# Kernel optimization log

Measured on AMD Instinct MI355X. Metric: run time of the kernel, lower is better.

## Reference

```python
import jax, jax.numpy as jnp
import numpy as np

N = 20000      # nodes / tokens
H = 256        # hidden_size
NH = 8         # num_heads
HD = NH * H    # num_heads * hidden_size = 2048
EPS = 1e-5


def setup_inputs() -> dict:
    key = jax.random.key(0)
    ks = jax.random.split(key, 24)

    def lin_w(k, i, o):
        # xavier-ish scale for a Linear weight stored as [in, out]
        return jax.random.normal(k, (i, o), jnp.float32) * (1.0 / np.sqrt(i))

    inp = {
        'q': jax.random.normal(ks[0], (N, H), jnp.float32),
        'k': jax.random.normal(ks[1], (N, H), jnp.float32),
        'v': jax.random.normal(ks[2], (N, H), jnp.float32),
        'layer': 1,
        'Wq1': lin_w(ks[3], H, HD), 'bq1': jnp.zeros((HD,), jnp.float32),
        'Wk1': lin_w(ks[4], H, HD), 'bk1': jnp.zeros((HD,), jnp.float32),
        'Wq2': lin_w(ks[5], H, HD), 'bq2': jnp.zeros((HD,), jnp.float32),
        'Wk2': lin_w(ks[6], H, HD), 'bk2': jnp.zeros((HD,), jnp.float32),
        'Wv':  lin_w(ks[7], H, HD), 'bv':  jnp.zeros((HD,), jnp.float32),
        'ln_g': jnp.ones((HD,), jnp.float32),
        'ln_b': jnp.zeros((HD,), jnp.float32),
        'Wo': lin_w(ks[8], HD, H), 'bo': jnp.zeros((H,), jnp.float32),
        'lq1': jax.random.normal(ks[9], (H,), jnp.float32) * 0.1,
        'lk1': jax.random.normal(ks[10], (H,), jnp.float32) * 0.1,
        'lq2': jax.random.normal(ks[11], (H,), jnp.float32) * 0.1,
        'lk2': jax.random.normal(ks[12], (H,), jnp.float32) * 0.1,
    }
    return inp


def reference(q, k, v, layer, Wq1, bq1, Wk1, bk1, Wq2, bq2, Wk2, bk2,
              Wv, bv, ln_g, ln_b, Wo, bo, lq1, lk1, lq2, lk2):
    # projections: [N, H] -> [N, HD]
    q1 = q @ Wq1 + bq1
    k1 = k @ Wk1 + bk1
    q2 = q @ Wq2 + bq2
    k2 = k @ Wk2 + bk2
    vv = v @ Wv + bv

    # linear attention: K^T V -> [HD, HD]  (dropout is identity in eval mode)
    k1v = k1.T @ vv
    k2v = k2.T @ vv

    # lambda gating (scalars)
    lam1 = jnp.exp(jnp.sum(lq1 * lk1))
    lam2 = jnp.exp(jnp.sum(lq2 * lk2))
    lam_init = 0.8 - 0.6 * jnp.exp(jnp.asarray(-0.3 * layer, jnp.float32))
    lam_full = lam1 - lam2 + lam_init

    # Q @ (K^T V), differential subtraction: [N, HD]
    x = q1 @ k1v - lam_full * (q2 @ k2v)

    # LayerNorm over last dim (biased variance, eps=1e-5, like torch)
    mu = jnp.mean(x, axis=-1, keepdims=True)
    var = jnp.mean(jnp.square(x - mu), axis=-1, keepdims=True)
    x = (x - mu) / jnp.sqrt(var + EPS) * ln_g + ln_b

    x = x * (1.0 - lam_init)
    return x @ Wo + bo  # [N, H]
```

## Files before the change

### kernel.cpp

```cpp
#include <hip/hip_runtime.h>
#include <stdint.h>

typedef __bf16 bf16x8 __attribute__((ext_vector_type(8)));
typedef __bf16 bf16x4v __attribute__((ext_vector_type(4)));
typedef float f32x4 __attribute__((ext_vector_type(4)));
typedef float f32x2 __attribute__((ext_vector_type(2)));
typedef unsigned short u16x4 __attribute__((ext_vector_type(4)));
typedef unsigned short u16x8 __attribute__((ext_vector_type(8)));

#define NTOK 20000
#define NTP  20480
#define HIW  256
#define HD   2048
#define LDKP 66
#define LDS2 72
#define TSZ  16384

static __device__ __forceinline__ float bf2f(unsigned short h) {
  union { unsigned u; float f; } c; c.u = ((unsigned)h) << 16;
  return c.f;
}
static __device__ __forceinline__ unsigned short fbits(float x) {
  __bf16 h = (__bf16)x;
  return __builtin_bit_cast(unsigned short, h);
}

#define WRED(x) { x += __shfl_xor(x,32); x += __shfl_xor(x,16); x += __shfl_xor(x,8); \
                  x += __shfl_xor(x,4);  x += __shfl_xor(x,2);  x += __shfl_xor(x,1); }


__global__ __launch_bounds__(256) void k_front(
    const float* __restrict__ kk, const float* __restrict__ vv,
    const float* __restrict__ Wq1, const float* __restrict__ Wk1,
    const float* __restrict__ Wq2, const float* __restrict__ Wk2,
    const float* __restrict__ lq1, const float* __restrict__ lk1,
    const float* __restrict__ lq2, const float* __restrict__ lk2,
    const float* __restrict__ bq1, const float* __restrict__ bk1,
    const float* __restrict__ bq2, const float* __restrict__ bk2,
    const int* __restrict__ layer,
    unsigned short* __restrict__ kT, unsigned short* __restrict__ vT,
    float* __restrict__ skp, float* __restrict__ svp,
    unsigned short* __restrict__ Pc_part, float* __restrict__ scal,
    float* __restrict__ S) {
  __shared__ float SMEM[64][260];
  const int b = blockIdx.x, t = threadIdx.x;

  if (b < 640) {
    const int tile = b >> 1, m = b & 1;
    const float* src = m ? vv : kk;
    unsigned short* dstT = m ? vT : kT;
    float* sump = m ? svp : skp;
    #pragma unroll
    for (int i = 0; i < 16; ++i) {
      int ch = i * 256 + t;
      int row = ch >> 6, c4 = (ch & 63) * 4;
      int gtok = tile * 64 + row;
      f32x4 val = {0.f, 0.f, 0.f, 0.f};
      if (gtok < NTOK) val = *(const f32x4*)&src[(size_t)gtok * HIW + c4];
      *(f32x4*)&SMEM[row][c4] = val;
    }
    __syncthreads();
    float sum = 0.f;
    unsigned short cv[64];
    #pragma unroll
    for (int tok = 0; tok < 64; ++tok) {
      float x = SMEM[tok][t];
      sum += x;
      cv[tok] = fbits(x);
    }
    sump[tile * 256 + t] = sum;
    size_t base = (size_t)tile * TSZ + (size_t)t * 64;
    #pragma unroll
    for (int s = 0; s < 8; ++s)
      *(u16x8*)&dstT[base + s * 8] = *(const u16x8*)&cv[s * 8];
  } else if (b < 768) {
    unsigned short* Ak = (unsigned short*)SMEM;
    unsigned short* Bk = Ak + 128 * LDKP;
    const int idx = b - 640;
    const int pair = idx >> 6, rem = idx & 63;
    const int z = rem & 15, by = (rem >> 4) & 1, bx = (rem >> 5) & 1;
    const int i0 = bx * 128, j0 = by * 128;
    const int lane = t & 63, wave = t >> 6;
    const int wr = (wave >> 1) * 64, wc = (wave & 1) * 64;
    const int r15 = lane & 15, kg = (lane >> 4) * 8;
    const float* Wa = pair ? Wq2 : Wq1;
    const float* Wb = pair ? Wk2 : Wk1;
    f32x4 acc[4][4];
    #pragma unroll
    for (int m = 0; m < 4; ++m)
      #pragma unroll
      for (int n = 0; n < 4; ++n) acc[m][n] = (f32x4){0.f, 0.f, 0.f, 0.f};
    const int srow = t >> 1, sh = (t & 1) * 32;
    for (int kt = 0; kt < 2; ++kt) {
      const int kb = z * 128 + kt * 64 + sh;
      __syncthreads();
      #pragma unroll
      for (int c = 0; c < 8; ++c) {
        f32x4 a = *(const f32x4*)&Wa[(size_t)(i0 + srow) * HD + kb + c * 4];
        f32x4 bb = *(const f32x4*)&Wb[(size_t)(j0 + srow) * HD + kb + c * 4];
        bf16x4v oa, ob;
        #pragma unroll
        for (int u = 0; u < 4; ++u) { oa[u] = (__bf16)a[u]; ob[u] = (__bf16)bb[u]; }
        *(bf16x4v*)&Ak[srow * LDKP + sh + c * 4] = oa;
        *(bf16x4v*)&Bk[srow * LDKP + sh + c * 4] = ob;
      }
      __syncthreads();
      #pragma unroll
      for (int ks = 0; ks < 2; ++ks) {
        const int ko = ks * 32 + kg;
        bf16x8 ah[4], bh[4];
        #pragma unroll
        for (int m = 0; m < 4; ++m)
          ah[m] = *(const bf16x8*)&Ak[(wr + m * 16 + r15) * LDKP + ko];
        #pragma unroll
        for (int n = 0; n < 4; ++n)
          bh[n] = *(const bf16x8*)&Bk[(wc + n * 16 + r15) * LDKP + ko];
        #pragma unroll
        for (int m = 0; m < 4; ++m)
          #pragma unroll
          for (int n = 0; n < 4; ++n)
            acc[m][n] = __builtin_amdgcn_mfma_f32_16x16x32_bf16(ah[m], bh[n], acc[m][n], 0, 0, 0);
      }
    }
    const int rg = (lane >> 4) * 4;
    unsigned short* Pp = Pc_part + (size_t)(pair * 16 + z) * 65536;
    #pragma unroll
    for (int m = 0; m < 4; ++m)
      #pragma unroll
      for (int n = 0; n < 4; ++n)
        #pragma unroll
        for (int r = 0; r < 4; ++r)
          Pp[(i0 + wr + m * 16 + rg + r) * 256 + (j0 + wc + n * 16 + r15)] = fbits(acc[m][n][r]);
  } else if (b == 768) {
    float* red = (float*)SMEM;
    float p1 = lq1[t] * lk1[t], p2 = lq2[t] * lk2[t];
    float d1 = 0.f, d2 = 0.f;
    #pragma unroll
    for (int u = 0; u < 8; ++u) {
      d1 += bq1[t * 8 + u] * bk1[t * 8 + u];
      d2 += bq2[t * 8 + u] * bk2[t * 8 + u];
    }
    WRED(p1); WRED(p2); WRED(d1); WRED(d2);
    int w = t >> 6;
    if ((t & 63) == 0) { red[w] = p1; red[4 + w] = p2; red[8 + w] = d1; red[12 + w] = d2; }
    __syncthreads();
    if (t == 0) {
      float s1 = red[0] + red[1] + red[2] + red[3];
      float s2 = red[4] + red[5] + red[6] + red[7];
      float dd1 = red[8] + red[9] + red[10] + red[11];
      float dd2 = red[12] + red[13] + red[14] + red[15];
      float li = 0.8f - 0.6f * expf(-0.3f * (float)layer[0]);
      float lam = expf(s1) - expf(s2) + li;
      scal[0] = lam; scal[1] = -lam; scal[2] = 1.0f - li; scal[3] = li;
      scal[4] = dd1 - lam * dd2;
    }
  } else {
    const f32x4 z4 = {0.f, 0.f, 0.f, 0.f};
    #pragma unroll
    for (int i = 0; i < 64; ++i)
      *(f32x4*)&S[i * 1024 + t * 4] = z4;
  }
}

__global__ __launch_bounds__(512) void k_mid(
    const unsigned short* __restrict__ kT, const unsigned short* __restrict__ vT,
    float* __restrict__ S, const unsigned short* __restrict__ Pc_part,
    const float* __restrict__ skp, const float* __restrict__ svp,
    float* __restrict__ Pc, float* __restrict__ sk, float* __restrict__ sv,
    const float* __restrict__ Wk1, const float* __restrict__ Wk2,
    const float* __restrict__ Wq1, const float* __restrict__ Wq2,
    const float* __restrict__ bq1, const float* __restrict__ bq2,
    const float* __restrict__ bk1, const float* __restrict__ bk2,
    const float* __restrict__ scal, float* __restrict__ gc, float* __restrict__ uc) {
  __shared__ unsigned short SB[2 * 2 * 128 * LDS2];
  const int b = blockIdx.x, t = threadIdx.x;

  if (b < 256) {
    const int z = b & 63, by = (b >> 6) & 1, bx = (b >> 7) & 1;
    const int i0 = bx * 128, j0 = by * 128;
    const int lane = t & 63, wave = t >> 6;
    const int wr = (wave >> 1) * 32, wc = (wave & 1) * 64;
    const int r15 = lane & 15, kg = (lane >> 4) * 8;
    const int m = t >> 8;
    const int local = t & 255;
    const int row2 = local >> 1;
    const int koff = (local & 1) * 32;
    const unsigned short* srcT = m ? vT : kT;
    const size_t tbase = (size_t)(5 * z) * TSZ + (size_t)((m ? j0 : i0) + row2) * 64 + koff;
    const int lds_off = m * 128 * LDS2 + row2 * LDS2 + koff;

    f32x4 acc[2][4];
    #pragma unroll
    for (int mm = 0; mm < 2; ++mm)
      #pragma unroll
      for (int n = 0; n < 4; ++n) acc[mm][n] = (f32x4){0.f, 0.f, 0.f, 0.f};
    u16x8 rA[4], rB[4];

#define LOADT(R, KT)                                                          \
    { _Pragma("unroll")                                                       \
      for (int c = 0; c < 4; ++c)                                             \
        R[c] = *(const u16x8*)&srcT[tbase + (size_t)(KT) * TSZ + c * 8]; }
#define WRITET(BUF, R)                                                        \
    { unsigned short* d = &SB[(BUF) * 2 * 128 * LDS2 + lds_off];              \
      _Pragma("unroll")                                                       \
      for (int c = 0; c < 4; ++c) *(u16x8*)&d[c * 8] = R[c]; }

    LOADT(rA, 0)
    WRITET(0, rA)
    LOADT(rB, 1)
    asm volatile("s_waitcnt lgkmcnt(0)" ::: "memory");
    __builtin_amdgcn_s_barrier();

    #pragma unroll
    for (int kt = 0; kt < 5; ++kt) {
      const unsigned short* Ab = &SB[(kt & 1) * 2 * 128 * LDS2];
      const unsigned short* Bb = Ab + 128 * LDS2;
      __builtin_amdgcn_s_setprio(1);
      #pragma unroll
      for (int ks = 0; ks < 2; ++ks) {
        const int ko = ks * 32 + kg;
        bf16x8 ah[2], bh[4];
        #pragma unroll
        for (int mm = 0; mm < 2; ++mm)
          ah[mm] = *(const bf16x8*)&Ab[(wr + mm * 16 + r15) * LDS2 + ko];
        #pragma unroll
        for (int n = 0; n < 4; ++n)
          bh[n] = *(const bf16x8*)&Bb[(wc + n * 16 + r15) * LDS2 + ko];
        #pragma unroll
        for (int mm = 0; mm < 2; ++mm)
          #pragma unroll
          for (int n = 0; n < 4; ++n)
            acc[mm][n] = __builtin_amdgcn_mfma_f32_16x16x32_bf16(ah[mm], bh[n], acc[mm][n], 0, 0, 0);
      }
      __builtin_amdgcn_s_setprio(0);
      if (kt < 4) {
        if ((kt & 1) == 0) {
          WRITET(1, rB)
          if (kt + 2 <= 4) LOADT(rA, kt + 2)
        } else {
          WRITET(0, rA)
          if (kt + 2 <= 4) LOADT(rB, kt + 2)
        }
      }
      asm volatile("s_waitcnt lgkmcnt(0)" ::: "memory");
      __builtin_amdgcn_s_barrier();
    }
#undef LOADT
#undef WRITET
    const int rg = (lane >> 4) * 4;
    #pragma unroll
    for (int mm = 0; mm < 2; ++mm)
      #pragma unroll
      for (int n = 0; n < 4; ++n)
        #pragma unroll
        for (int r = 0; r < 4; ++r)
          atomicAdd(&S[(i0 + wr + mm * 16 + rg + r) * 256 + (j0 + wc + n * 16 + r15)],
                    acc[mm][n][r]);
  } else if (b < 288) {
    if (t < 256) {
      size_t idx = (size_t)(b - 256) * 2048 + t * 8;
      float s1[8] = {}, s2[8] = {};
      #pragma unroll 2
      for (int z = 0; z < 16; ++z) {
        u16x8 ha = *(const u16x8*)&Pc_part[(size_t)z * 65536 + idx];
        u16x8 hb = *(const u16x8*)&Pc_part[(size_t)(16 + z) * 65536 + idx];
        #pragma unroll
        for (int u = 0; u < 8; ++u) { s1[u] += bf2f(ha[u]); s2[u] += bf2f(hb[u]); }
      }
      float lam = scal[0];
      #pragma unroll
      for (int u = 0; u < 8; ++u) Pc[idx + u] = s1[u] - lam * s2[u];
    }
  } else if (b < 290) {
    if (t < 256) {
      const float* src = (b == 288) ? skp : svp;
      float s = 0.f;
      for (int z = 0; z < 320; ++z) s += src[z * 256 + t];
      if (b == 288) sk[t] = s; else sv[t] = s;
    }
  } else {
    if (t < 256) {
      int bb = b - 290, lane = t & 63, w = t >> 6;
      bool dogc = bb < 16;
      const float* A1 = dogc ? Wk1 : Wq1;
      const float* A2 = dogc ? Wk2 : Wq2;
      const float* x1 = dogc ? bq1 : bk1;
      const float* x2 = dogc ? bq2 : bk2;
      float* outv = dogc ? gc : uc;
      float lam = scal[0];
      int rb = (bb & 15) * 16 + w * 4;
      for (int q2 = 0; q2 < 4; ++q2) {
        int row = rb + q2;
        float s1 = 0.f, s2 = 0.f;
        #pragma unroll
        for (int c = 0; c < 8; ++c) {
          int kk2 = c * 256 + lane * 4;
          f32x4 a1 = *(const f32x4*)&A1[(size_t)row * HD + kk2];
          f32x4 a2 = *(const f32x4*)&A2[(size_t)row * HD + kk2];
          f32x4 v1 = *(const f32x4*)&x1[kk2];
          f32x4 v2 = *(const f32x4*)&x2[kk2];
          #pragma unroll
          for (int u = 0; u < 4; ++u) { s1 += a1[u] * v1[u]; s2 += a2[u] * v2[u]; }
        }
        WRED(s1); WRED(s2);
        if (lane == 0) outv[row] = s1 - lam * s2;
      }
    }
  }
}

__global__ __launch_bounds__(256) void k_ac(
    const float* __restrict__ Pc, const float* __restrict__ S,
    const float* __restrict__ gc, const float* __restrict__ sk,
    float* __restrict__ Ac, float* __restrict__ tc, float* __restrict__ rv,
    float* __restrict__ scal) {
  int b = blockIdx.x, t = threadIdx.x;
  if (b < 32) {
    __shared__ float Pt[32][68];
    __shared__ float St[64][68];
    int i0 = (b >> 2) * 32, j0 = (b & 3) * 64;
    int ti = t >> 5, tj = t & 31;
    float acc[4][2] = {};
    for (int kt = 0; kt < 256; kt += 64) {
      __syncthreads();
      {
        int rr = t >> 3, c8 = (t & 7) * 8;
        *(f32x4*)&Pt[rr][c8] = *(const f32x4*)&Pc[(i0 + rr) * 256 + kt + c8];
        *(f32x4*)&Pt[rr][c8 + 4] = *(const f32x4*)&Pc[(i0 + rr) * 256 + kt + c8 + 4];
      }
      {
        int rr = t >> 2, c16 = (t & 3) * 16;
        #pragma unroll
        for (int c = 0; c < 4; ++c)
          *(f32x4*)&St[rr][c16 + c * 4] = *(const f32x4*)&S[(kt + rr) * 256 + j0 + c16 + c * 4];
      }
      __syncthreads();
      #pragma unroll 8
      for (int k2 = 0; k2 < 64; ++k2) {
        float a[4];
        #pragma unroll
        for (int u = 0; u < 4; ++u) a[u] = Pt[ti * 4 + u][k2];
        f32x2 b2 = *(const f32x2*)&St[k2][tj * 2];
        #pragma unroll
        for (int u = 0; u < 4; ++u) { acc[u][0] += a[u] * b2[0]; acc[u][1] += a[u] * b2[1]; }
      }
    }
    #pragma unroll
    for (int u = 0; u < 4; ++u) {
      Ac[(i0 + ti * 4 + u) * 256 + j0 + tj * 2] = acc[u][0];
      Ac[(i0 + ti * 4 + u) * 256 + j0 + tj * 2 + 1] = acc[u][1];
    }
  } else if (b == 32) {
    int lane = t & 63, w = t >> 6;
    f32x4 sk4 = *(const f32x4*)&sk[lane * 4];
    for (int ii = 0; ii < 64; ++ii) {
      int i = w * 64 + ii;
      f32x4 p4 = *(const f32x4*)&Pc[i * 256 + lane * 4];
      float s = p4[0] * sk4[0] + p4[1] * sk4[1] + p4[2] * sk4[2] + p4[3] * sk4[3];
      WRED(s);
      if (lane == 0) tc[i] = s;
    }
  } else {
    float s0 = 0.f, s1 = 0.f, s2 = 0.f, s3 = 0.f;
    #pragma unroll 4
    for (int i = 0; i < 256; i += 4) {
      s0 += gc[i] * S[i * 256 + t];
      s1 += gc[i + 1] * S[(i + 1) * 256 + t];
      s2 += gc[i + 2] * S[(i + 2) * 256 + t];
      s3 += gc[i + 3] * S[(i + 3) * 256 + t];
    }
    rv[t] = (s0 + s1) + (s2 + s3);
    if (t < 64) {
      f32x4 g4 = *(const f32x4*)&gc[t * 4];
      f32x4 sk4 = *(const f32x4*)&sk[t * 4];
      float a = g4[0] * sk4[0] + g4[1] * sk4[1] + g4[2] * sk4[2] + g4[3] * sk4[3];
      WRED(a);
      if (t == 0) scal[5] = a;
    }
  }
}

__global__ __launch_bounds__(256) void k_gc(
    const float* __restrict__ Ac, const float* __restrict__ Wv,
    const float* __restrict__ tc, const float* __restrict__ uc,
    const float* __restrict__ sv, const float* __restrict__ rv,
    const float* __restrict__ bv, const float* __restrict__ scal,
    float* __restrict__ Gc, float* __restrict__ cc) {
  __shared__ float At[64][68];
  __shared__ float Bt[64][132];
  __shared__ float svr[256], rvr[256];
  int t = threadIdx.x;
  int i0 = blockIdx.x * 64, j0 = blockIdx.y * 128;
  int ti = t >> 5, tj = t & 31;
  svr[t] = sv[t]; rvr[t] = rv[t];
  float acc[8][4] = {};
  f32x4 swa = {0.f, 0.f, 0.f, 0.f}, sca = {0.f, 0.f, 0.f, 0.f};
  for (int kt = 0; kt < 256; kt += 64) {
    __syncthreads();
    {
      int rr = t >> 2, c16 = (t & 3) * 16;
      #pragma unroll
      for (int c = 0; c < 4; ++c)
        *(f32x4*)&At[rr][c16 + c * 4] = *(const f32x4*)&Ac[(i0 + rr) * 256 + kt + c16 + c * 4];
    }
    {
      int rr = t >> 2, c32 = (t & 3) * 32;
      #pragma unroll
      for (int c = 0; c < 8; ++c)
        *(f32x4*)&Bt[rr][c32 + c * 4] = *(const f32x4*)&Wv[(size_t)(kt + rr) * HD + j0 + c32 + c * 4];
    }
    __syncthreads();
    #pragma unroll 8
    for (int k2 = 0; k2 < 64; ++k2) {
      float a[8];
      #pragma unroll
      for (int u = 0; u < 8; ++u) a[u] = At[ti * 8 + u][k2];
      f32x4 b = *(const f32x4*)&Bt[k2][tj * 4];
      float svk = svr[kt + k2], rvk = rvr[kt + k2];
      swa += b * svk; sca += b * rvk;
      #pragma unroll
      for (int u = 0; u < 8; ++u)
        #pragma unroll
        for (int v = 0; v < 4; ++v) acc[u][v] += a[u] * b[v];
    }
  }
  int j = j0 + tj * 4;
  f32x4 bv4 = *(const f32x4*)&bv[j];
  f32x4 wnb;
  #pragma unroll
  for (int v = 0; v < 4; ++v) wnb[v] = swa[v] + 20000.0f * bv4[v];
  if (blockIdx.x == 0 && ti == 0) {
    float ac = scal[5], dc = scal[4];
    f32x4 ccv;
    #pragma unroll
    for (int v = 0; v < 4; ++v) ccv[v] = sca[v] + ac * bv4[v] + dc * wnb[v];
    *(f32x4*)&cc[j] = ccv;
  }
  #pragma unroll
  for (int u = 0; u < 8; ++u) {
    int i = i0 + ti * 8 + u;
    float tci = tc[i], uci = uc[i];
    f32x4 o;
    #pragma unroll
    for (int v = 0; v < 4; ++v)
      o[v] = acc[u][v] + tci * bv4[v] + uci * wnb[v];
    *(f32x4*)&Gc[(size_t)i * HD + j] = o;
  }
}

__global__ __launch_bounds__(256) void k_post(
    const float* __restrict__ Gc, const float* __restrict__ cc,
    const float* __restrict__ Wo, const float* __restrict__ g,
    const float* __restrict__ lnb, const float* __restrict__ scal_c,
    unsigned short* __restrict__ Bt2, float* __restrict__ M_part,
    float* __restrict__ Hc_part, float* __restrict__ scal) {
  __shared__ float SMEM[8768];
  int b = blockIdx.x, t = threadIdx.x;
  if (b < 17) {
    int lane = t & 63, w = t >> 6;
    if (b < 16) {
      int rb = b * 16 + w * 4;
      for (int q2 = 0; q2 < 4; ++q2) {
        int row = rb + q2;
        float s1 = 0.f, s2 = 0.f;
        #pragma unroll
        for (int c = 0; c < 8; ++c) {
          int kk2 = c * 256 + lane * 4;
          f32x4 g4 = *(const f32x4*)&Gc[(size_t)row * HD + kk2];
          f32x4 c4v = *(const f32x4*)&cc[kk2];
          #pragma unroll
          for (int u = 0; u < 4; ++u) { s1 += g4[u]; s2 += g4[u] * c4v[u]; }
        }
        WRED(s1); WRED(s2);
        if (lane == 0) {
          int base = ((256 + (row >> 5)) * 64 + ((row >> 3) & 3) * 16) * 8 + (row & 7);
          Bt2[base] = fbits(s1 * (1.0f / 2048.0f));
          Bt2[base + 8] = fbits(s2);
        }
      }
    } else {
      float s1 = 0.f, s2 = 0.f;
      #pragma unroll
      for (int c = 0; c < 2; ++c) {
        f32x4 v = *(const f32x4*)&cc[t * 8 + c * 4];
        #pragma unroll
        for (int u = 0; u < 4; ++u) { s1 += v[u]; s2 += v[u] * v[u]; }
      }
      WRED(s1); WRED(s2);
      if ((t & 63) == 0) { SMEM[t >> 6] = s1; SMEM[4 + (t >> 6)] = s2; }
      __syncthreads();
      if (t == 0) {
        scal[6] = SMEM[4] + SMEM[5] + SMEM[6] + SMEM[7];
        scal[7] = (SMEM[0] + SMEM[1] + SMEM[2] + SMEM[3]) * (1.0f / 2048.0f);
      }
      for (int idx = t; idx < 14 * 256; idx += 256) {
        int ci = idx >> 8, kk2 = idx & 255;
        int col = 514 + ci;
        Bt2[((256 + (kk2 >> 5)) * 64 + ((kk2 >> 3) & 3) * 16 + (col & 15)) * 8 + (kk2 & 7)] = 0;
      }
    }
  } else if (b < 81) {
    float (*Gi)[68] = (float(*)[68])SMEM;
    float (*Gj)[69] = (float(*)[69])(SMEM + 64 * 68);
    int idx = b - 17;
    int bx = idx & 3, by = (idx >> 2) & 3, z = idx >> 4;
    int i0 = bx * 64, j0 = by * 64;
    int ti = t >> 5, tj = t & 31;
    float acc[8][2] = {};
    for (int kt = 0; kt < 512; kt += 64) {
      int kb = z * 512 + kt;
      __syncthreads();
      {
        int rr = t >> 2, c16 = (t & 3) * 16;
        #pragma unroll
        for (int c = 0; c < 4; ++c) {
          *(f32x4*)&Gi[rr][c16 + c * 4] = *(const f32x4*)&Gc[(size_t)(i0 + rr) * HD + kb + c16 + c * 4];
          *(f32x4*)&Gj[rr][c16 + c * 4] = *(const f32x4*)&Gc[(size_t)(j0 + rr) * HD + kb + c16 + c * 4];
        }
      }
      __syncthreads();
      #pragma unroll 8
      for (int k2 = 0; k2 < 64; ++k2) {
        float a[8];
        #pragma unroll
        for (int u = 0; u < 8; ++u) a[u] = Gi[ti * 8 + u][k2];
        float b0 = Gj[tj * 2][k2], b1 = Gj[tj * 2 + 1][k2];
        #pragma unroll
        for (int u = 0; u < 8; ++u) { acc[u][0] += a[u] * b0; acc[u][1] += a[u] * b1; }
      }
    }
    #pragma unroll
    for (int u = 0; u < 8; ++u) {
      M_part[(size_t)z * 65536 + (i0 + ti * 8 + u) * 256 + j0 + tj * 2] = acc[u][0];
      M_part[(size_t)z * 65536 + (i0 + ti * 8 + u) * 256 + j0 + tj * 2 + 1] = acc[u][1];
    }
  } else {
    float (*At)[68] = (float(*)[68])SMEM;
    float (*Bt)[68] = (float(*)[68])(SMEM + 32 * 68);
    int idx = b - 81;
    int bx = idx % 9, rem = idx / 9, by = rem & 3, z = rem >> 2;
    int i0 = bx * 32, j0 = by * 64;
    float s2 = scal_c[2];
    int ti = t >> 5, tj = t & 31;
    float acc[4][2] = {};
    for (int kt = 0; kt < 512; kt += 64) {
      int kb = z * 512 + kt;
      __syncthreads();
      {
        int rr = t >> 3, c8 = (t & 7) * 8, gi = i0 + rr;
        #pragma unroll
        for (int h = 0; h < 8; h += 4) {
          f32x4 g4 = *(const f32x4*)&g[kb + c8 + h];
          f32x4 a;
          if (gi < 256) {
            f32x4 gg = *(const f32x4*)&Gc[(size_t)gi * HD + kb + c8 + h];
            #pragma unroll
            for (int u = 0; u < 4; ++u) a[u] = gg[u] * g4[u];
          } else if (gi == 256) {
            a = g4;
          } else if (gi == 257) {
            f32x4 c4v = *(const f32x4*)&cc[kb + c8 + h];
            #pragma unroll
            for (int u = 0; u < 4; ++u) a[u] = c4v[u] * g4[u];
          } else if (gi == 258) {
            a = *(const f32x4*)&lnb[kb + c8 + h];
          } else {
            a = (f32x4){0.f, 0.f, 0.f, 0.f};
          }
          *(f32x4*)&At[rr][c8 + h] = a;
        }
      }
      {
        int rr = t >> 2, c16 = (t & 3) * 16;
        #pragma unroll
        for (int c = 0; c < 4; ++c) {
          f32x4 bb = *(const f32x4*)&Wo[(size_t)(kb + rr) * 256 + j0 + c16 + c * 4];
          #pragma unroll
          for (int u = 0; u < 4; ++u) bb[u] *= s2;
          *(f32x4*)&Bt[rr][c16 + c * 4] = bb;
        }
      }
      __syncthreads();
      #pragma unroll 8
      for (int k2 = 0; k2 < 64; ++k2) {
        float a[4];
        #pragma unroll
        for (int u = 0; u < 4; ++u) a[u] = At[ti * 4 + u][k2];
        f32x2 b2 = *(const f32x2*)&Bt[k2][tj * 2];
        #pragma unroll
        for (int u = 0; u < 4; ++u) { acc[u][0] += a[u] * b2[0]; acc[u][1] += a[u] * b2[1]; }
      }
    }
    #pragma unroll
    for (int u = 0; u < 4; ++u) {
      Hc_part[(size_t)z * 73728 + (i0 + ti * 4 + u) * 256 + j0 + tj * 2] = acc[u][0];
      Hc_part[(size_t)z * 73728 + (i0 + ti * 4 + u) * 256 + j0 + tj * 2 + 1] = acc[u][1];
    }
  }
}

__global__ __launch_bounds__(256) void k_red2(
    const float* __restrict__ M_part, const float* __restrict__ Hc_part,
    const float* __restrict__ bo, unsigned short* __restrict__ Bt2,
    float* __restrict__ wbar, float* __restrict__ hcv, float* __restrict__ bcv) {
  int bi = blockIdx.x, z2 = blockIdx.y, t = threadIdx.x;
  if (z2 == 2) {
    if (bi != 0) return;
    float s0 = 0.f, s1 = 0.f, s2 = 0.f;
    #pragma unroll
    for (int z = 0; z < 4; ++z) {
      s0 += Hc_part[(size_t)z * 73728 + 256 * 256 + t];
      s1 += Hc_part[(size_t)z * 73728 + 257 * 256 + t];
      s2 += Hc_part[(size_t)z * 73728 + 258 * 256 + t];
    }
    wbar[t] = s0; hcv[t] = s1; bcv[t] = s2 + bo[t];
    return;
  }
  __shared__ unsigned short T[64][256];
  const float* src = z2 ? Hc_part : M_part;
  const size_t sp = z2 ? 73728 : 65536;
  const int base = z2 ? 256 : 0;
  for (int ii = 0; ii < 64; ++ii) {
    int i = bi * 64 + ii;
    float s = 0.f;
    #pragma unroll
    for (int z = 0; z < 4; ++z) s += src[z * sp + i * 256 + t];
    T[ii][t] = fbits(s);
  }
  __syncthreads();
  const int col = base + t;
  #pragma unroll
  for (int c = 0; c < 64; c += 8) {
    u16x8 o;
    #pragma unroll
    for (int u = 0; u < 8; ++u) o[u] = T[c + u][t];
    int kk0 = bi * 64 + c;
    int addr = (((col >> 4) * 8 + (kk0 >> 5)) * 64 + ((kk0 >> 3) & 3) * 16 + (col & 15)) * 8;
    *(u16x8*)&Bt2[addr] = o;
  }
}

__global__ __launch_bounds__(512) void k_out(
    const float* __restrict__ q, const unsigned short* __restrict__ Bt2,
    const float* __restrict__ hcv, const float* __restrict__ wbar,
    const float* __restrict__ bcv, const float* __restrict__ scal,
    float* __restrict__ out) {
  __shared__ unsigned short As[32 * 264];
  __shared__ float zbuf[32][260];
  __shared__ float sqp[4][32];
  __shared__ float muL[32], m2L[32];
  const int t = threadIdx.x, lane = t & 63, wave = t >> 6;
  const int row0 = blockIdx.x * 32;
  const int r15 = lane & 15, kg = lane >> 4;
  {
    #pragma unroll
    for (int i = 0; i < 4; ++i) {
      int ch = i * 512 + t;
      int row = ch >> 6, c4 = (ch & 63) * 4;
      f32x4 v = *(const f32x4*)&q[(size_t)(row0 + row) * HIW + c4];
      bf16x4v o;
      #pragma unroll
      for (int u = 0; u < 4; ++u) o[u] = (__bf16)v[u];
      *(bf16x4v*)&As[row * 264 + c4] = o;
    }
  }
  __syncthreads();
  const bool isM = wave < 4;
  const int wcol = isM ? wave * 64 : 256 + (wave - 4) * 64;
  const int grp0 = wcol >> 4;
  f32x4 acc[2][5];
  #pragma unroll
  for (int m = 0; m < 2; ++m)
    #pragma unroll
    for (int n = 0; n < 5; ++n) acc[m][n] = (f32x4){0.f, 0.f, 0.f, 0.f};
  __builtin_amdgcn_s_setprio(1);
  #pragma unroll
  for (int ko = 0; ko < 8; ++ko) {
    bf16x8 af0 = *(const bf16x8*)&As[r15 * 264 + ko * 32 + kg * 8];
    bf16x8 af1 = *(const bf16x8*)&As[(16 + r15) * 264 + ko * 32 + kg * 8];
    #pragma unroll
    for (int ni = 0; ni < 5; ++ni) {
      if (ni == 4 && wave != 7) continue;
      const int grp = (ni == 4) ? 32 : grp0 + ni;
      bf16x8 bfr = *(const bf16x8*)&Bt2[(size_t)(grp * 8 + ko) * 512 + lane * 8];
      acc[0][ni] = __builtin_amdgcn_mfma_f32_16x16x32_bf16(af0, bfr, acc[0][ni], 0, 0, 0);
      acc[1][ni] = __builtin_amdgcn_mfma_f32_16x16x32_bf16(af1, bfr, acc[1][ni], 0, 0, 0);
    }
  }
  __builtin_amdgcn_s_setprio(0);
  if (isM) {
    #pragma unroll
    for (int m = 0; m < 2; ++m)
      #pragma unroll
      for (int r = 0; r < 4; ++r) {
        int rowl = m * 16 + kg * 4 + r;
        float p = 0.f;
        #pragma unroll
        for (int ni = 0; ni < 4; ++ni) {
          int col = wcol + ni * 16 + r15;
          p += acc[m][ni][r] * bf2f(As[rowl * 264 + col]);
        }
        p += __shfl_xor(p, 1); p += __shfl_xor(p, 2);
        p += __shfl_xor(p, 4); p += __shfl_xor(p, 8);
        if (r15 == 0) sqp[wave][rowl] = p;
      }
  } else {
    #pragma unroll
    for (int m = 0; m < 2; ++m)
      #pragma unroll
      for (int r = 0; r < 4; ++r) {
        int rowl = m * 16 + kg * 4 + r;
        #pragma unroll
        for (int ni = 0; ni < 4; ++ni)
          zbuf[rowl][(wcol - 256) + ni * 16 + r15] = acc[m][ni][r];
      }
    if (wave == 7) {
      #pragma unroll
      for (int m = 0; m < 2; ++m)
        #pragma unroll
        for (int r = 0; r < 4; ++r) {
          int rowl = m * 16 + kg * 4 + r;
          if (r15 == 0) muL[rowl] = acc[m][4][r];
          if (r15 == 1) m2L[rowl] = acc[m][4][r];
        }
    }
  }
  __syncthreads();
  const float css = scal[6], cbar = scal[7];
  #pragma unroll
  for (int i = 0; i < 4; ++i) {
    const int row = i * 8 + wave;
    const int c4 = lane * 4;
    float mu = muL[row] + cbar;
    float ss = (sqp[0][row] + sqp[1][row]) + (sqp[2][row] + sqp[3][row]) +
               2.0f * m2L[row] + css;
    float var = ss * (1.0f / 2048.0f) - mu * mu;
    float rstd = rsqrtf(var + 1e-5f);
    f32x4 zv = *(const f32x4*)&zbuf[row][c4];
    f32x4 h4 = *(const f32x4*)&hcv[c4];
    f32x4 w4 = *(const f32x4*)&wbar[c4];
    f32x4 b4 = *(const f32x4*)&bcv[c4];
    f32x4 o;
    #pragma unroll
    for (int u = 0; u < 4; ++u)
      o[u] = rstd * (zv[u] + h4[u] - mu * w4[u]) + b4[u];
    *(f32x4*)&out[(size_t)(row0 + row) * HIW + c4] = o;
  }
}

extern "C" void kernel_launch(void* const* d_in, const int* in_sizes, int n_in,
                              void* d_out, int out_size, void* d_ws, size_t ws_size,
                              hipStream_t stream) {
  const float* q   = (const float*)d_in[0];
  const float* k   = (const float*)d_in[1];
  const float* v   = (const float*)d_in[2];
  const int* layer = (const int*)d_in[3];
  const float* Wq1 = (const float*)d_in[4];  const float* bq1 = (const float*)d_in[5];
  const float* Wk1 = (const float*)d_in[6];  const float* bk1 = (const float*)d_in[7];
  const float* Wq2 = (const float*)d_in[8];  const float* bq2 = (const float*)d_in[9];
  const float* Wk2 = (const float*)d_in[10]; const float* bk2 = (const float*)d_in[11];
  const float* Wv  = (const float*)d_in[12]; const float* bv  = (const float*)d_in[13];
  const float* lng = (const float*)d_in[14]; const float* lnb = (const float*)d_in[15];
  const float* Wo  = (const float*)d_in[16]; const float* bo  = (const float*)d_in[17];
  const float* lq1 = (const float*)d_in[18]; const float* lk1 = (const float*)d_in[19];
  const float* lq2 = (const float*)d_in[20]; const float* lk2 = (const float*)d_in[21];

  char* p = (char*)d_ws;
  unsigned short* kT = (unsigned short*)p;
  float* M_part  = (float*)p;
  float* Hc_part = (float*)(p + 1048576);
  unsigned short* Bt2 = (unsigned short*)(p + 1048576 + 1179648);
  p += (size_t)256 * NTP * 2;
  unsigned short* vT = (unsigned short*)p;
  float* Gc = (float*)p;
  p += (size_t)256 * NTP * 2;
  float* skp = (float*)p;     p += (size_t)320 * 256 * 4;
  float* svp = (float*)p;     p += (size_t)320 * 256 * 4;
  unsigned short* Pc_part = (unsigned short*)p; p += (size_t)32 * 65536 * 2;
  float* S  = (float*)p;      p += 65536 * 4;
  float* Pc = (float*)p;      p += 65536 * 4;
  float* sk = (float*)p;      p += 1024;
  float* sv = (float*)p;      p += 1024;
  float* gc = (float*)p;      p += 1024;
  float* uc = (float*)p;      p += 1024;
  float* tc = (float*)p;      p += 1024;
  float* rv = (float*)p;      p += 1024;
  float* cc = (float*)p;      p += 2048 * 4;
  float* Ac = (float*)p;      p += 65536 * 4;
  float* wbar = (float*)p;    p += 1024;
  float* hcv  = (float*)p;    p += 1024;
  float* bcv  = (float*)p;    p += 1024;
  float* scal = (float*)p;    p += 256;

  const dim3 b256(256);
  k_front<<<dim3(770), b256, 0, stream>>>(k, v, Wq1, Wk1, Wq2, Wk2,
      lq1, lk1, lq2, lk2, bq1, bk1, bq2, bk2, layer, kT, vT, skp, svp, Pc_part, scal, S);
  k_mid<<<dim3(322), dim3(512), 0, stream>>>(kT, vT, S, Pc_part, skp, svp, Pc, sk, sv,
      Wk1, Wk2, Wq1, Wq2, bq1, bq2, bk1, bk2, scal, gc, uc);
  k_ac<<<dim3(34), b256, 0, stream>>>(Pc, S, gc, sk, Ac, tc, rv, scal);
  k_gc<<<dim3(4, 16), b256, 0, stream>>>(Ac, Wv, tc, uc, sv, rv, bv, scal, Gc, cc);
  k_post<<<dim3(225), b256, 0, stream>>>(Gc, cc, Wo, lng, lnb, scal, Bt2, M_part, Hc_part, scal);
  k_red2<<<dim3(4, 3), b256, 0, stream>>>(M_part, Hc_part, bo, Bt2, wbar, hcv, bcv);
  k_out<<<dim3(625), dim3(512), 0, stream>>>(q, Bt2, hcv, wbar, bcv, scal, (float*)d_out);
}
```

Baseline: 172.7 us.

## Remove split-K partials, fuse k_red2 into k_post, store zbuf as bf16

Drops the split-K decomposition in the Wq·Wk product blocks of k_front and in the Gram/Wo blocks of k_post. Each block now runs the full K loop and writes final results directly: fp32 partial pairs for Pc, and bf16 into the swizzled Bt2 layout plus the wbar/hcv/bcv vectors. This removes the k_red2 launch and the large partial-sum buffers. The cost is far fewer blocks (8 instead of 128, and 52 instead of 208), each with much longer serial K loops, which risks underusing the GPU on those stages. k_out also keeps its zbuf in bf16 to cut LDS use, at some precision cost.

```diff
diff --git a/kernel.cpp b/kernel.cpp
--- a/kernel.cpp
+++ b/kernel.cpp
@@ -24,10 +24,12 @@
   __bf16 h = (__bf16)x;
   return __builtin_bit_cast(unsigned short, h);
 }
+static __device__ __forceinline__ int bt2_addr(int col, int kk) {
+  return (((col >> 4) * 8 + (kk >> 5)) * 64 + ((kk >> 3) & 3) * 16 + (col & 15)) * 8 + (kk & 7);
+}
 
 #define WRED(x) { x += __shfl_xor(x,32); x += __shfl_xor(x,16); x += __shfl_xor(x,8); \
                   x += __shfl_xor(x,4);  x += __shfl_xor(x,2);  x += __shfl_xor(x,1); }
-
 
 __global__ __launch_bounds__(256) void k_front(
     const float* __restrict__ kk, const float* __restrict__ vv,
@@ -40,7 +42,7 @@
     const int* __restrict__ layer,
     unsigned short* __restrict__ kT, unsigned short* __restrict__ vT,
     float* __restrict__ skp, float* __restrict__ svp,
-    unsigned short* __restrict__ Pc_part, float* __restrict__ scal,
+    float* __restrict__ Pc_part, float* __restrict__ scal,
     float* __restrict__ S) {
   __shared__ float SMEM[64][260];
   const int b = blockIdx.x, t = threadIdx.x;
@@ -73,12 +75,11 @@
     #pragma unroll
     for (int s = 0; s < 8; ++s)
       *(u16x8*)&dstT[base + s * 8] = *(const u16x8*)&cv[s * 8];
-  } else if (b < 768) {
+  } else if (b < 648) {
     unsigned short* Ak = (unsigned short*)SMEM;
     unsigned short* Bk = Ak + 128 * LDKP;
     const int idx = b - 640;
-    const int pair = idx >> 6, rem = idx & 63;
-    const int z = rem & 15, by = (rem >> 4) & 1, bx = (rem >> 5) & 1;
+    const int pair = idx >> 2, bx = (idx >> 1) & 1, by = idx & 1;
     const int i0 = bx * 128, j0 = by * 128;
     const int lane = t & 63, wave = t >> 6;
     const int wr = (wave >> 1) * 64, wc = (wave & 1) * 64;
@@ -91,8 +92,8 @@
       #pragma unroll
       for (int n = 0; n < 4; ++n) acc[m][n] = (f32x4){0.f, 0.f, 0.f, 0.f};
     const int srow = t >> 1, sh = (t & 1) * 32;
-    for (int kt = 0; kt < 2; ++kt) {
-      const int kb = z * 128 + kt * 64 + sh;
+    for (int kt = 0; kt < 32; ++kt) {
+      const int kb = kt * 64 + sh;
       __syncthreads();
       #pragma unroll
       for (int c = 0; c < 8; ++c) {
@@ -123,15 +124,15 @@
       }
     }
     const int rg = (lane >> 4) * 4;
-    unsigned short* Pp = Pc_part + (size_t)(pair * 16 + z) * 65536;
+    float* Pp = Pc_part + (size_t)pair * 65536;
     #pragma unroll
     for (int m = 0; m < 4; ++m)
       #pragma unroll
       for (int n = 0; n < 4; ++n)
         #pragma unroll
         for (int r = 0; r < 4; ++r)
-          Pp[(i0 + wr + m * 16 + rg + r) * 256 + (j0 + wc + n * 16 + r15)] = fbits(acc[m][n][r]);
-  } else if (b == 768) {
+          Pp[(i0 + wr + m * 16 + rg + r) * 256 + (j0 + wc + n * 16 + r15)] = acc[m][n][r];
+  } else if (b == 648) {
     float* red = (float*)SMEM;
     float p1 = lq1[t] * lk1[t], p2 = lq2[t] * lk2[t];
     float d1 = 0.f, d2 = 0.f;
@@ -164,7 +165,7 @@
 
 __global__ __launch_bounds__(512) void k_mid(
     const unsigned short* __restrict__ kT, const unsigned short* __restrict__ vT,
-    float* __restrict__ S, const unsigned short* __restrict__ Pc_part,
+    float* __restrict__ S, const float* __restrict__ Pc_part,
     const float* __restrict__ skp, const float* __restrict__ svp,
     float* __restrict__ Pc, float* __restrict__ sk, float* __restrict__ sv,
     const float* __restrict__ Wk1, const float* __restrict__ Wk2,
@@ -259,17 +260,16 @@
   } else if (b < 288) {
     if (t < 256) {
       size_t idx = (size_t)(b - 256) * 2048 + t * 8;
-      float s1[8] = {}, s2[8] = {};
-      #pragma unroll 2
-      for (int z = 0; z < 16; ++z) {
-        u16x8 ha = *(const u16x8*)&Pc_part[(size_t)z * 65536 + idx];
-        u16x8 hb = *(const u16x8*)&Pc_part[(size_t)(16 + z) * 65536 + idx];
-        #pragma unroll
-        for (int u = 0; u < 8; ++u) { s1[u] += bf2f(ha[u]); s2[u] += bf2f(hb[u]); }
-      }
       float lam = scal[0];
       #pragma unroll
-      for (int u = 0; u < 8; ++u) Pc[idx + u] = s1[u] - lam * s2[u];
+      for (int h = 0; h < 2; ++h) {
+        f32x4 p0 = *(const f32x4*)&Pc_part[idx + h * 4];
+        f32x4 p1 = *(const f32x4*)&Pc_part[65536 + idx + h * 4];
+        f32x4 o;
+        #pragma unroll
+        for (int u = 0; u < 4; ++u) o[u] = p0[u] - lam * p1[u];
+        *(f32x4*)&Pc[idx + h * 4] = o;
+      }
     }
   } else if (b < 290) {
     if (t < 256) {
@@ -451,9 +451,11 @@
 __global__ __launch_bounds__(256) void k_post(
     const float* __restrict__ Gc, const float* __restrict__ cc,
     const float* __restrict__ Wo, const float* __restrict__ g,
-    const float* __restrict__ lnb, const float* __restrict__ scal_c,
-    unsigned short* __restrict__ Bt2, float* __restrict__ M_part,
-    float* __restrict__ Hc_part, float* __restrict__ scal) {
+    const float* __restrict__ lnb, const float* __restrict__ bo,
+    const float* __restrict__ scal_c,
+    unsigned short* __restrict__ Bt2,
+    float* __restrict__ wbar, float* __restrict__ hcv, float* __restrict__ bcv,
+    float* __restrict__ scal) {
   __shared__ float SMEM[8768];
   int b = blockIdx.x, t = threadIdx.x;
   if (b < 17) {
@@ -473,9 +475,8 @@
         }
         WRED(s1); WRED(s2);
         if (lane == 0) {
-          int base = ((256 + (row >> 5)) * 64 + ((row >> 3) & 3) * 16) * 8 + (row & 7);
-          Bt2[base] = fbits(s1 * (1.0f / 2048.0f));
-          Bt2[base + 8] = fbits(s2);
+          Bt2[bt2_addr(512, row)] = fbits(s1 * (1.0f / 2048.0f));
+          Bt2[bt2_addr(513, row)] = fbits(s2);
         }
       }
     } else {
@@ -495,27 +496,25 @@
       }
       for (int idx = t; idx < 14 * 256; idx += 256) {
         int ci = idx >> 8, kk2 = idx & 255;
-        int col = 514 + ci;
-        Bt2[((256 + (kk2 >> 5)) * 64 + ((kk2 >> 3) & 3) * 16 + (col & 15)) * 8 + (kk2 & 7)] = 0;
-      }
-    }
-  } else if (b < 81) {
+        Bt2[bt2_addr(514 + ci, kk2)] = 0;
+      }
+    }
+  } else if (b < 33) {
     float (*Gi)[68] = (float(*)[68])SMEM;
     float (*Gj)[69] = (float(*)[69])(SMEM + 64 * 68);
     int idx = b - 17;
-    int bx = idx & 3, by = (idx >> 2) & 3, z = idx >> 4;
+    int bx = idx & 3, by = idx >> 2;
     int i0 = bx * 64, j0 = by * 64;
     int ti = t >> 5, tj = t & 31;
     float acc[8][2] = {};
-    for (int kt = 0; kt < 512; kt += 64) {
-      int kb = z * 512 + kt;
+    for (int kt = 0; kt < 2048; kt += 64) {
       __syncthreads();
       {
         int rr = t >> 2, c16 = (t & 3) * 16;
         #pragma unroll
         for (int c = 0; c < 4; ++c) {
-          *(f32x4*)&Gi[rr][c16 + c * 4] = *(const f32x4*)&Gc[(size_t)(i0 + rr) * HD + kb + c16 + c * 4];
-          *(f32x4*)&Gj[rr][c16 + c * 4] = *(const f32x4*)&Gc[(size_t)(j0 + rr) * HD + kb + c16 + c * 4];
+          *(f32x4*)&Gi[rr][c16 + c * 4] = *(const f32x4*)&Gc[(size_t)(i0 + rr) * HD + kt + c16 + c * 4];
+          *(f32x4*)&Gj[rr][c16 + c * 4] = *(const f32x4*)&Gc[(size_t)(j0 + rr) * HD + kt + c16 + c * 4];
         }
       }
       __syncthreads();
@@ -531,39 +530,39 @@
     }
     #pragma unroll
     for (int u = 0; u < 8; ++u) {
-      M_part[(size_t)z * 65536 + (i0 + ti * 8 + u) * 256 + j0 + tj * 2] = acc[u][0];
-      M_part[(size_t)z * 65536 + (i0 + ti * 8 + u) * 256 + j0 + tj * 2 + 1] = acc[u][1];
+      int i = i0 + ti * 8 + u;
+      Bt2[bt2_addr(j0 + tj * 2, i)]     = fbits(acc[u][0]);
+      Bt2[bt2_addr(j0 + tj * 2 + 1, i)] = fbits(acc[u][1]);
     }
   } else {
     float (*At)[68] = (float(*)[68])SMEM;
     float (*Bt)[68] = (float(*)[68])(SMEM + 32 * 68);
-    int idx = b - 81;
-    int bx = idx % 9, rem = idx / 9, by = rem & 3, z = rem >> 2;
+    int idx = b - 33;
+    int bx = idx % 9, by = idx / 9;
     int i0 = bx * 32, j0 = by * 64;
     float s2 = scal_c[2];
     int ti = t >> 5, tj = t & 31;
     float acc[4][2] = {};
-    for (int kt = 0; kt < 512; kt += 64) {
-      int kb = z * 512 + kt;
+    for (int kt = 0; kt < 2048; kt += 64) {
       __syncthreads();
       {
         int rr = t >> 3, c8 = (t & 7) * 8, gi = i0 + rr;
         #pragma unroll
         for (int h = 0; h < 8; h += 4) {
-          f32x4 g4 = *(const f32x4*)&g[kb + c8 + h];
+          f32x4 g4 = *(const f32x4*)&g[kt + c8 + h];
           f32x4 a;
           if (gi < 256) {
-            f32x4 gg = *(const f32x4*)&Gc[(size_t)gi * HD + kb + c8 + h];
+            f32x4 gg = *(const f32x4*)&Gc[(size_t)gi * HD + kt + c8 + h];
             #pragma unroll
             for (int u = 0; u < 4; ++u) a[u] = gg[u] * g4[u];
           } else if (gi == 256) {
             a = g4;
           } else if (gi == 257) {
-            f32x4 c4v = *(const f32x4*)&cc[kb + c8 + h];
+            f32x4 c4v = *(const f32x4*)&cc[kt + c8 + h];
             #pragma unroll
             for (int u = 0; u < 4; ++u) a[u] = c4v[u] * g4[u];
           } else if (gi == 258) {
-            a = *(const f32x4*)&lnb[kb + c8 + h];
+            a = *(const f32x4*)&lnb[kt + c8 + h];
           } else {
             a = (f32x4){0.f, 0.f, 0.f, 0.f};
           }
@@ -574,7 +573,7 @@
         int rr = t >> 2, c16 = (t & 3) * 16;
         #pragma unroll
         for (int c = 0; c < 4; ++c) {
-          f32x4 bb = *(const f32x4*)&Wo[(size_t)(kb + rr) * 256 + j0 + c16 + c * 4];
+          f32x4 bb = *(const f32x4*)&Wo[(size_t)(kt + rr) * 256 + j0 + c16 + c * 4];
           #pragma unroll
           for (int u = 0; u < 4; ++u) bb[u] *= s2;
           *(f32x4*)&Bt[rr][c16 + c * 4] = bb;
@@ -593,50 +592,19 @@
     }
     #pragma unroll
     for (int u = 0; u < 4; ++u) {
-      Hc_part[(size_t)z * 73728 + (i0 + ti * 4 + u) * 256 + j0 + tj * 2] = acc[u][0];
-      Hc_part[(size_t)z * 73728 + (i0 + ti * 4 + u) * 256 + j0 + tj * 2 + 1] = acc[u][1];
-    }
-  }
-}
-
-__global__ __launch_bounds__(256) void k_red2(
-    const float* __restrict__ M_part, const float* __restrict__ Hc_part,
-    const float* __restrict__ bo, unsigned short* __restrict__ Bt2,
-    float* __restrict__ wbar, float* __restrict__ hcv, float* __restrict__ bcv) {
-  int bi = blockIdx.x, z2 = blockIdx.y, t = threadIdx.x;
-  if (z2 == 2) {
-    if (bi != 0) return;
-    float s0 = 0.f, s1 = 0.f, s2 = 0.f;
-    #pragma unroll
-    for (int z = 0; z < 4; ++z) {
-      s0 += Hc_part[(size_t)z * 73728 + 256 * 256 + t];
-      s1 += Hc_part[(size_t)z * 73728 + 257 * 256 + t];
-      s2 += Hc_part[(size_t)z * 73728 + 258 * 256 + t];
-    }
-    wbar[t] = s0; hcv[t] = s1; bcv[t] = s2 + bo[t];
-    return;
-  }
-  __shared__ unsigned short T[64][256];
-  const float* src = z2 ? Hc_part : M_part;
-  const size_t sp = z2 ? 73728 : 65536;
-  const int base = z2 ? 256 : 0;
-  for (int ii = 0; ii < 64; ++ii) {
-    int i = bi * 64 + ii;
-    float s = 0.f;
-    #pragma unroll
-    for (int z = 0; z < 4; ++z) s += src[z * sp + i * 256 + t];
-    T[ii][t] = fbits(s);
-  }
-  __syncthreads();
-  const int col = base + t;
-  #pragma unroll
-  for (int c = 0; c < 64; c += 8) {
-    u16x8 o;
-    #pragma unroll
-    for (int u = 0; u < 8; ++u) o[u] = T[c + u][t];
-    int kk0 = bi * 64 + c;
-    int addr = (((col >> 4) * 8 + (kk0 >> 5)) * 64 + ((kk0 >> 3) & 3) * 16 + (col & 15)) * 8;
-    *(u16x8*)&Bt2[addr] = o;
+      int i = i0 + ti * 4 + u;
+      int j = j0 + tj * 2;
+      if (i < 256) {
+        Bt2[bt2_addr(256 + j, i)]     = fbits(acc[u][0]);
+        Bt2[bt2_addr(256 + j + 1, i)] = fbits(acc[u][1]);
+      } else if (i == 256) {
+        wbar[j] = acc[u][0]; wbar[j + 1] = acc[u][1];
+      } else if (i == 257) {
+        hcv[j] = acc[u][0]; hcv[j + 1] = acc[u][1];
+      } else if (i == 258) {
+        bcv[j] = acc[u][0] + bo[j]; bcv[j + 1] = acc[u][1] + bo[j + 1];
+      }
+    }
   }
 }
 
@@ -646,7 +614,7 @@
     const float* __restrict__ bcv, const float* __restrict__ scal,
     float* __restrict__ out) {
   __shared__ unsigned short As[32 * 264];
-  __shared__ float zbuf[32][260];
+  __shared__ unsigned short zbuf[32][264];
   __shared__ float sqp[4][32];
   __shared__ float muL[32], m2L[32];
   const int t = threadIdx.x, lane = t & 63, wave = t >> 6;
@@ -712,7 +680,7 @@
         int rowl = m * 16 + kg * 4 + r;
         #pragma unroll
         for (int ni = 0; ni < 4; ++ni)
-          zbuf[rowl][(wcol - 256) + ni * 16 + r15] = acc[m][ni][r];
+          zbuf[rowl][(wcol - 256) + ni * 16 + r15] = fbits(acc[m][ni][r]);
       }
     if (wave == 7) {
       #pragma unroll
@@ -736,14 +704,14 @@
                2.0f * m2L[row] + css;
     float var = ss * (1.0f / 2048.0f) - mu * mu;
     float rstd = rsqrtf(var + 1e-5f);
-    f32x4 zv = *(const f32x4*)&zbuf[row][c4];
+    u16x4 zh = *(const u16x4*)&zbuf[row][c4];
     f32x4 h4 = *(const f32x4*)&hcv[c4];
     f32x4 w4 = *(const f32x4*)&wbar[c4];
     f32x4 b4 = *(const f32x4*)&bcv[c4];
     f32x4 o;
     #pragma unroll
     for (int u = 0; u < 4; ++u)
-      o[u] = rstd * (zv[u] + h4[u] - mu * w4[u]) + b4[u];
+      o[u] = rstd * (bf2f(zh[u]) + h4[u] - mu * w4[u]) + b4[u];
     *(f32x4*)&out[(size_t)(row0 + row) * HIW + c4] = o;
   }
 }
@@ -767,16 +735,14 @@
 
   char* p = (char*)d_ws;
   unsigned short* kT = (unsigned short*)p;
-  float* M_part  = (float*)p;
-  float* Hc_part = (float*)(p + 1048576);
-  unsigned short* Bt2 = (unsigned short*)(p + 1048576 + 1179648);
+  unsigned short* Bt2 = (unsigned short*)p;
   p += (size_t)256 * NTP * 2;
   unsigned short* vT = (unsigned short*)p;
   float* Gc = (float*)p;
   p += (size_t)256 * NTP * 2;
   float* skp = (float*)p;     p += (size_t)320 * 256 * 4;
   float* svp = (float*)p;     p += (size_t)320 * 256 * 4;
-  unsigned short* Pc_part = (unsigned short*)p; p += (size_t)32 * 65536 * 2;
+  float* Pc_part = (float*)p; p += (size_t)2 * 65536 * 4;
   float* S  = (float*)p;      p += 65536 * 4;
   float* Pc = (float*)p;      p += 65536 * 4;
   float* sk = (float*)p;      p += 1024;
@@ -793,13 +759,13 @@
   float* scal = (float*)p;    p += 256;
 
   const dim3 b256(256);
-  k_front<<<dim3(770), b256, 0, stream>>>(k, v, Wq1, Wk1, Wq2, Wk2,
+  k_front<<<dim3(650), b256, 0, stream>>>(k, v, Wq1, Wk1, Wq2, Wk2,
       lq1, lk1, lq2, lk2, bq1, bk1, bq2, bk2, layer, kT, vT, skp, svp, Pc_part, scal, S);
   k_mid<<<dim3(322), dim3(512), 0, stream>>>(kT, vT, S, Pc_part, skp, svp, Pc, sk, sv,
       Wk1, Wk2, Wq1, Wq2, bq1, bq2, bk1, bk2, scal, gc, uc);
   k_ac<<<dim3(34), b256, 0, stream>>>(Pc, S, gc, sk, Ac, tc, rv, scal);
   k_gc<<<dim3(4, 16), b256, 0, stream>>>(Ac, Wv, tc, uc, sv, rv, bv, scal, Gc, cc);
-  k_post<<<dim3(225), b256, 0, stream>>>(Gc, cc, Wo, lng, lnb, scal, Bt2, M_part, Hc_part, scal);
-  k_red2<<<dim3(4, 3), b256, 0, stream>>>(M_part, Hc_part, bo, Bt2, wbar, hcv, bcv);
+  k_post<<<dim3(69), b256, 0, stream>>>(Gc, cc, Wo, lng, lnb, bo, scal, Bt2,
+                                        wbar, hcv, bcv, scal);
   k_out<<<dim3(625), dim3(512), 0, stream>>>(q, Bt2, hcv, wbar, bcv, scal, (float*)d_out);
 }
```

Result: slower. 421.7 us (+144.2%).
